# Performance work log

Hardware: AMD Instinct MI355X
Metric: run time of the kernel (lower is better)

## Reference

```python
import jax, jax.numpy as jnp
import numpy as np

B, S, D = 2, 2048, 1024
H = 16
HD = D // H
MLP = 4096
EPS = 1e-5


def _layernorm(x, g, b):
    mu = jnp.mean(x, axis=-1, keepdims=True)
    var = jnp.mean(jnp.square(x - mu), axis=-1, keepdims=True)
    return (x - mu) * jax.lax.rsqrt(var + EPS) * g + b


def setup_inputs() -> dict:
    key = jax.random.key(0)
    ks = jax.random.split(key, 16)
    sd = 0.02
    return {
        "x": jax.random.normal(ks[0], (B, S, D), jnp.float32),
        "dis_attn_mask": jax.random.normal(ks[1], (B, S, S), jnp.float32) * 0.1,
        "cls_attn_mask": jax.random.normal(ks[2], (B, S, S), jnp.float32) * 0.1,
        "wq": jax.random.normal(ks[3], (D, D), jnp.float32) * sd,
        "bq": jnp.zeros((D,), jnp.float32),
        "wk": jax.random.normal(ks[4], (D, D), jnp.float32) * sd,
        "bk": jnp.zeros((D,), jnp.float32),
        "wv": jax.random.normal(ks[5], (D, D), jnp.float32) * sd,
        "bv": jnp.zeros((D,), jnp.float32),
        "ln1_g": jnp.ones((D,), jnp.float32),
        "ln1_b": jnp.zeros((D,), jnp.float32),
        "ln2_g": jnp.ones((D,), jnp.float32),
        "ln2_b": jnp.zeros((D,), jnp.float32),
        "w1": jax.random.normal(ks[6], (D, MLP), jnp.float32) * sd,
        "b1": jnp.zeros((MLP,), jnp.float32),
        "w2": jax.random.normal(ks[7], (MLP, D), jnp.float32) * sd,
        "b2": jnp.zeros((D,), jnp.float32),
    }


def reference(x, dis_attn_mask, cls_attn_mask, wq, bq, wk, bk, wv, bv,
              ln1_g, ln1_b, ln2_g, ln2_b, w1, b1, w2, b2):
    res = x
    h = _layernorm(x, ln1_g, ln1_b)
    q = h @ wq + bq
    k = h @ wk + bk
    v = h @ wv + bv
    # NOTE: original torch code uses .view(B, H, S, HD) on a contiguous
    # [B, S, D] tensor (no transpose); row-major reshape reproduces this.
    q = q.reshape(B, H, S, HD)
    k = k.reshape(B, H, S, HD)
    v = v.reshape(B, H, S, HD)
    w = jnp.einsum('bhsd,bhtd->bhst', q, k) * (HD ** -0.5)
    w = w + dis_attn_mask[:, None] + cls_attn_mask[:, None]
    w = jax.nn.softmax(w, axis=-1)
    h_attn = jnp.einsum('bhst,bhtd->bhsd', w, v).reshape(B, S, D)
    h = h_attn + res
    h = _layernorm(h, ln2_g, ln2_b)
    res2 = h
    h = jax.nn.gelu(h @ w1 + b1, approximate=False) @ w2 + b2
    return h + res2
```

## Files before the change

kernel.cpp:

```cpp
#include <hip/hip_runtime.h>
#include <hip/hip_bf16.h>
#include <math.h>

#define BB 2
#define SS 2048
#define DD 1024
#define HH 16
#define MLPD 4096

typedef __attribute__((ext_vector_type(8))) short bf16x8;
typedef __attribute__((ext_vector_type(4))) float f32x4;
typedef __attribute__((ext_vector_type(4))) unsigned short us4;

static __device__ __forceinline__ float fast_exp2(float x) {
#if __has_builtin(__builtin_amdgcn_exp2f)
  return __builtin_amdgcn_exp2f(x);
#else
  return exp2f(x);
#endif
}
static __device__ __forceinline__ float fast_rcp(float x) {
#if __has_builtin(__builtin_amdgcn_rcpf)
  return __builtin_amdgcn_rcpf(x);
#else
  return 1.0f / x;
#endif
}

static __device__ __forceinline__ unsigned short f2bf(float f) {
  union { float f; unsigned int u; } v; v.f = f;
  unsigned int r = v.u + 0x7fffu + ((v.u >> 16) & 1u);
  return (unsigned short)(r >> 16);
}
static __device__ __forceinline__ float bf2f(unsigned short b) {
  return __uint_as_float(((unsigned int)b) << 16);
}

static __device__ __forceinline__ float gelu_f(float x) {
  float u = x * x;
  float z = x * fmaf(u, 0.0713548162f, 1.59576912f);
  float e = fast_exp2(z * -1.44269504f);
  return x * fast_rcp(1.0f + e);
}

static __device__ __forceinline__ int swz(int row) {
  return (row & 3) ^ ((row >> 2) & 3);
}

__global__ __launch_bounds__(256) void transpose_to_bf16(
    const float* __restrict__ src, unsigned short* __restrict__ dst,
    int K, int N) {
  __shared__ float tile[32][33];
  int t = threadIdx.x;
  int c = t & 31, rl = t >> 5;
  int bx = blockIdx.x, by = blockIdx.y;
#pragma unroll
  for (int i = 0; i < 4; ++i) {
    int row = rl * 4 + i;
    tile[row][c] = src[(size_t)(by * 32 + row) * N + bx * 32 + c];
  }
  __syncthreads();
#pragma unroll
  for (int i = 0; i < 4; ++i) {
    int n = rl * 4 + i;
    dst[(size_t)(bx * 32 + n) * K + by * 32 + c] = f2bf(tile[c][n]);
  }
}

__global__ __launch_bounds__(256) void transpose_qkv(
    const float* __restrict__ wq, const float* __restrict__ wk,
    const float* __restrict__ wv, unsigned short* __restrict__ dst) {
  __shared__ float tile[32][33];
  const float* src = blockIdx.z == 0 ? wq : blockIdx.z == 1 ? wk : wv;
  unsigned short* d = dst + (size_t)blockIdx.z * 1024 * 1024;
  int t = threadIdx.x;
  int c = t & 31, rl = t >> 5;
  int bx = blockIdx.x, by = blockIdx.y;
#pragma unroll
  for (int i = 0; i < 4; ++i) {
    int row = rl * 4 + i;
    tile[row][c] = src[(size_t)(by * 32 + row) * DD + bx * 32 + c];
  }
  __syncthreads();
#pragma unroll
  for (int i = 0; i < 4; ++i) {
    int n = rl * 4 + i;
    d[(size_t)(bx * 32 + n) * DD + by * 32 + c] = f2bf(tile[c][n]);
  }
}

__global__ __launch_bounds__(256) void concat_bias(
    const float* __restrict__ bq, const float* __restrict__ bk,
    const float* __restrict__ bv, float* __restrict__ dst) {
  int i = blockIdx.x * 256 + threadIdx.x;
  if (i < 1024) dst[i] = bq[i];
  else if (i < 2048) dst[i] = bk[i - 1024];
  else if (i < 3072) dst[i] = bv[i - 2048];
}

__global__ __launch_bounds__(256) void mask_prep(
    const float* __restrict__ dis, const float* __restrict__ cls,
    unsigned short* __restrict__ cm) {
  size_t i = ((size_t)blockIdx.x * 256 + threadIdx.x) * 4;
  float4 d = *(const float4*)(dis + i);
  float4 c = *(const float4*)(cls + i);
  us4 o;
  o[0] = f2bf((d.x + c.x) * 1.44269504f);
  o[1] = f2bf((d.y + c.y) * 1.44269504f);
  o[2] = f2bf((d.z + c.z) * 1.44269504f);
  o[3] = f2bf((d.w + c.w) * 1.44269504f);
  *(us4*)(cm + i) = o;
}

template <bool BF_IN, bool ADD>
__global__ __launch_bounds__(256) void ln_bf16(
    const void* __restrict__ in, const float* __restrict__ add,
    const float* __restrict__ g, const float* __restrict__ beta,
    unsigned short* __restrict__ out) {
  int row = blockIdx.x;
  int t = threadIdx.x;
  float x[4];
  if (BF_IN) {
    us4 b4 = *(const us4*)((const unsigned short*)in + (size_t)row * DD + t * 4);
#pragma unroll
    for (int i = 0; i < 4; ++i) x[i] = bf2f(b4[i]);
  } else {
    float4 f4 = *(const float4*)((const float*)in + (size_t)row * DD + t * 4);
    x[0] = f4.x; x[1] = f4.y; x[2] = f4.z; x[3] = f4.w;
  }
  if (ADD) {
    float4 a4 = *(const float4*)(add + (size_t)row * DD + t * 4);
    x[0] += a4.x; x[1] += a4.y; x[2] += a4.z; x[3] += a4.w;
  }
  float s1 = x[0] + x[1] + x[2] + x[3];
  float s2 = x[0] * x[0] + x[1] * x[1] + x[2] * x[2] + x[3] * x[3];
#pragma unroll
  for (int off = 32; off > 0; off >>= 1) {
    s1 += __shfl_down(s1, off);
    s2 += __shfl_down(s2, off);
  }
  __shared__ float sa[4], sb[4];
  int wid = t >> 6;
  if ((t & 63) == 0) { sa[wid] = s1; sb[wid] = s2; }
  __syncthreads();
  s1 = sa[0] + sa[1] + sa[2] + sa[3];
  s2 = sb[0] + sb[1] + sb[2] + sb[3];
  float mean = s1 * (1.0f / 1024.0f);
  float var = s2 * (1.0f / 1024.0f) - mean * mean;
  float rstd = rsqrtf(var + 1e-5f);
  float4 gv = *(const float4*)(g + t * 4);
  float4 bv = *(const float4*)(beta + t * 4);
  us4 o;
  o[0] = f2bf((x[0] - mean) * rstd * gv.x + bv.x);
  o[1] = f2bf((x[1] - mean) * rstd * gv.y + bv.y);
  o[2] = f2bf((x[2] - mean) * rstd * gv.z + bv.z);
  o[3] = f2bf((x[3] - mean) * rstd * gv.w + bv.w);
  *(us4*)(out + (size_t)row * DD + t * 4) = o;
}

template <int BN, bool GELU, bool ADDSRC, bool OUT_BF16, bool SPLIT3>
__global__ __launch_bounds__(256) void gemm_bf16(
    const unsigned short* __restrict__ A, const unsigned short* __restrict__ BT,
    const float* __restrict__ bias, const unsigned short* __restrict__ addsrc,
    void* C0, void* C1, void* C2, int M, int N, int K) {
  constexpr int BJ = BN / 32;
  constexpr int BCH = BN / 64;
  __shared__ __align__(16) unsigned short As[128][32];
  __shared__ __align__(16) unsigned short Bs[BN][32];
  int tid = threadIdx.x;
  int wave = tid >> 6, lane = tid & 63;
  int g = lane >> 4, c16 = lane & 15;
  int m0 = blockIdx.y * 128, n0 = blockIdx.x * BN;
  int wm = (wave >> 1) * 64, wn = (wave & 1) * (BN / 2);
  int lrow = lane >> 2, lq = lane & 3;
  int dq = (lq ^ swz(lrow)) * 8;
  const unsigned short* aS = A + (size_t)(m0 + wave * 32 + lrow) * K + lq * 8;
  unsigned short* aD0 = &As[wave * 32 + lrow][dq];
  unsigned short* aD1 = &As[wave * 32 + 16 + lrow][dq];
  const unsigned short* bS = BT + (size_t)(n0 + wave * (BCH * 16) + lrow) * K + lq * 8;
  unsigned short* bD0 = &Bs[wave * (BCH * 16) + lrow][dq];
  unsigned short* bD1 = &Bs[(wave * (BCH * 16) + 16 + lrow) % BN][dq];
  int vA = (g ^ swz(c16)) * 8;
  const int KI = K / 32;
  const size_t rK = 16 * (size_t)K;

  bf16x8 a0a = *(const bf16x8*)(aS);
  bf16x8 a1a = *(const bf16x8*)(aS + rK);
  bf16x8 b0a = *(const bf16x8*)(bS);
  bf16x8 b1a;
  if constexpr (BCH == 2) b1a = *(const bf16x8*)(bS + rK);
  bf16x8 a0b = *(const bf16x8*)(aS + 32);
  bf16x8 a1b = *(const bf16x8*)(aS + rK + 32);
  bf16x8 b0b = *(const bf16x8*)(bS + 32);
  bf16x8 b1b;
  if constexpr (BCH == 2) b1b = *(const bf16x8*)(bS + rK + 32);

  f32x4 acc[4][BJ] = {};
  for (int kt = 0; kt < KI; kt += 2) {
    __syncthreads();
    *(bf16x8*)aD0 = a0a;
    *(bf16x8*)aD1 = a1a;
    *(bf16x8*)bD0 = b0a;
    if constexpr (BCH == 2) *(bf16x8*)bD1 = b1a;
    __syncthreads();
    if (kt + 2 < KI) {
      int ko = (kt + 2) * 32;
      a0a = *(const bf16x8*)(aS + ko);
      a1a = *(const bf16x8*)(aS + rK + ko);
      b0a = *(const bf16x8*)(bS + ko);
      if constexpr (BCH == 2) b1a = *(const bf16x8*)(bS + rK + ko);
    }
    {
      bf16x8 a[4], b[BJ];
#pragma unroll
      for (int i = 0; i < 4; ++i) a[i] = *(const bf16x8*)&As[wm + i * 16 + c16][vA];
#pragma unroll
      for (int j = 0; j < BJ; ++j) b[j] = *(const bf16x8*)&Bs[wn + j * 16 + c16][vA];
#pragma unroll
      for (int i = 0; i < 4; ++i)
#pragma unroll
        for (int j = 0; j < BJ; ++j)
          acc[i][j] = __builtin_amdgcn_mfma_f32_16x16x32_bf16(a[i], b[j], acc[i][j], 0, 0, 0);
    }
    __syncthreads();
    *(bf16x8*)aD0 = a0b;
    *(bf16x8*)aD1 = a1b;
    *(bf16x8*)bD0 = b0b;
    if constexpr (BCH == 2) *(bf16x8*)bD1 = b1b;
    __syncthreads();
    if (kt + 3 < KI) {
      int ko = (kt + 3) * 32;
      a0b = *(const bf16x8*)(aS + ko);
      a1b = *(const bf16x8*)(aS + rK + ko);
      b0b = *(const bf16x8*)(bS + ko);
      if constexpr (BCH == 2) b1b = *(const bf16x8*)(bS + rK + ko);
    }
    {
      bf16x8 a[4], b[BJ];
#pragma unroll
      for (int i = 0; i < 4; ++i) a[i] = *(const bf16x8*)&As[wm + i * 16 + c16][vA];
#pragma unroll
      for (int j = 0; j < BJ; ++j) b[j] = *(const bf16x8*)&Bs[wn + j * 16 + c16][vA];
#pragma unroll
      for (int i = 0; i < 4; ++i)
#pragma unroll
        for (int j = 0; j < BJ; ++j)
          acc[i][j] = __builtin_amdgcn_mfma_f32_16x16x32_bf16(a[i], b[j], acc[i][j], 0, 0, 0);
    }
  }
  unsigned short* dstb = nullptr;
  int lc0 = 0;
  if (SPLIT3) {
    int which = n0 >> 10;
    dstb = (unsigned short*)(which == 0 ? C0 : which == 1 ? C1 : C2);
    lc0 = n0 & 1023;
  }
#pragma unroll
  for (int j = 0; j < BJ; ++j) {
    int coff = wn + j * 16 + c16;
    float bj = bias[n0 + coff];
#pragma unroll
    for (int i = 0; i < 4; ++i) {
#pragma unroll
      for (int r = 0; r < 4; ++r) {
        int row = m0 + wm + i * 16 + g * 4 + r;
        float cval = acc[i][j][r] + bj;
        if (GELU) cval = gelu_f(cval);
        if (ADDSRC) cval += bf2f(addsrc[(size_t)row * N + n0 + coff]);
        if (SPLIT3) {
          dstb[(size_t)row * 1024 + lc0 + coff] = f2bf(cval);
        } else if (OUT_BF16) {
          ((unsigned short*)C0)[(size_t)row * N + n0 + coff] = f2bf(cval);
        } else {
          ((float*)C0)[(size_t)row * N + n0 + coff] = cval;
        }
      }
    }
  }
}

__global__ __launch_bounds__(512) void attn_mfma(
    const unsigned short* __restrict__ q, const unsigned short* __restrict__ k,
    const unsigned short* __restrict__ v, const unsigned short* __restrict__ cm,
    unsigned short* __restrict__ outO) {
  __shared__ __align__(16) unsigned short Ks[2][64][32];
  __shared__ __align__(16) unsigned short Vt[64][72];
  __shared__ __align__(16) unsigned short Ps[128][72];
  int tid = threadIdx.x;
  int wave = tid >> 6, lane = tid & 63;
  int g = lane >> 4, c16 = lane & 15;
  int qt = blockIdx.x, h = blockIdx.y, b = blockIdx.z;
  int s0 = qt * 128;
  int wr = wave * 16;
  size_t headoff = (size_t)b * SS * DD + (size_t)h * SS * 64;
  const unsigned short* qb = q + headoff;
  const unsigned short* kb = k + headoff;
  const unsigned short* vb = v + headoff;
  const unsigned short* cmb = cm + (size_t)b * SS * SS;

  int kkey = tid >> 3, kseg = tid & 7;
  unsigned short* kdst = &Ks[kseg >> 2][kkey][((kseg & 3) ^ swz(kkey)) * 8];
  const unsigned short* ksrc = kb + (size_t)kkey * 64 + kseg * 8;
  const unsigned short* vsrc = vb + (size_t)lane * 64 + wave * 8;
  int vK = (g ^ swz(c16)) * 8;

  bf16x8 qf0, qf1;
  {
    size_t qrow = (size_t)(s0 + wr + c16) * 64;
    qf0 = *(const bf16x8*)(qb + qrow + g * 8);
    qf1 = *(const bf16x8*)(qb + qrow + 32 + g * 8);
  }
  bf16x8 ones;
#pragma unroll
  for (int j = 0; j < 8; ++j) ones[j] = (short)0x3F80;
  f32x4 o[4] = {};
  f32x4 ol = {};
  const float scale2 = 0.18033688f;

  bf16x8 kreg = *(const bf16x8*)(ksrc);
  bf16x8 vreg = *(const bf16x8*)(vsrc);
  unsigned short cmc[4][4];
#pragma unroll
  for (int t = 0; t < 4; ++t)
#pragma unroll
    for (int r = 0; r < 4; ++r)
      cmc[t][r] = cmb[(size_t)(s0 + wr + g * 4 + r) * SS + t * 16 + c16];

  for (int kt = 0; kt < 32; ++kt) {
    __syncthreads();
    *(bf16x8*)kdst = kreg;
#pragma unroll
    for (int j = 0; j < 8; ++j) Vt[wave * 8 + j][lane] = (unsigned short)vreg[j];
    __syncthreads();

    int ktn = kt + 1 < 32 ? kt + 1 : 31;
    bf16x8 kregN = *(const bf16x8*)(ksrc + (size_t)ktn * 4096);
    bf16x8 vregN = *(const bf16x8*)(vsrc + (size_t)ktn * 4096);
    unsigned short cmN[4][4];
#pragma unroll
    for (int t = 0; t < 4; ++t)
#pragma unroll
      for (int r = 0; r < 4; ++r)
        cmN[t][r] = cmb[(size_t)(s0 + wr + g * 4 + r) * SS + ktn * 64 + t * 16 + c16];

    f32x4 s[4] = {};
#pragma unroll
    for (int t = 0; t < 4; ++t) {
      bf16x8 b0 = *(const bf16x8*)&Ks[0][t * 16 + c16][vK];
      bf16x8 b1 = *(const bf16x8*)&Ks[1][t * 16 + c16][vK];
      s[t] = __builtin_amdgcn_mfma_f32_16x16x32_bf16(qf0, b0, s[t], 0, 0, 0);
      s[t] = __builtin_amdgcn_mfma_f32_16x16x32_bf16(qf1, b1, s[t], 0, 0, 0);
    }
#pragma unroll
    for (int t = 0; t < 4; ++t)
#pragma unroll
      for (int r = 0; r < 4; ++r) {
        float p = fast_exp2(fmaf(s[t][r], scale2, bf2f(cmc[t][r])));
        Ps[wr + g * 4 + r][t * 16 + c16] = (unsigned short)(__float_as_uint(p) >> 16);
      }
#pragma unroll
    for (int ks = 0; ks < 2; ++ks) {
      bf16x8 pa = *(const bf16x8*)&Ps[wr + c16][ks * 32 + g * 8];
#pragma unroll
      for (int t2 = 0; t2 < 4; ++t2) {
        bf16x8 vb8 = *(const bf16x8*)&Vt[t2 * 16 + c16][ks * 32 + g * 8];
        o[t2] = __builtin_amdgcn_mfma_f32_16x16x32_bf16(pa, vb8, o[t2], 0, 0, 0);
      }
      ol = __builtin_amdgcn_mfma_f32_16x16x32_bf16(pa, ones, ol, 0, 0, 0);
    }
    kreg = kregN;
    vreg = vregN;
#pragma unroll
    for (int t = 0; t < 4; ++t)
#pragma unroll
      for (int r = 0; r < 4; ++r) cmc[t][r] = cmN[t][r];
  }
  float inv[4];
#pragma unroll
  for (int r = 0; r < 4; ++r) inv[r] = fast_rcp(ol[r]);
#pragma unroll
  for (int t2 = 0; t2 < 4; ++t2)
#pragma unroll
    for (int r = 0; r < 4; ++r) {
      int srow = s0 + wr + g * 4 + r;
      outO[headoff + (size_t)srow * 64 + t2 * 16 + c16] = f2bf(o[t2][r] * inv[r]);
    }
}

extern "C" void kernel_launch(void* const* d_in, const int* in_sizes, int n_in,
                              void* d_out, int out_size, void* d_ws, size_t ws_size,
                              hipStream_t stream) {
  const float* x    = (const float*)d_in[0];
  const float* dis  = (const float*)d_in[1];
  const float* cls  = (const float*)d_in[2];
  const float* wq   = (const float*)d_in[3];
  const float* bq   = (const float*)d_in[4];
  const float* wk   = (const float*)d_in[5];
  const float* bk   = (const float*)d_in[6];
  const float* wv   = (const float*)d_in[7];
  const float* bv   = (const float*)d_in[8];
  const float* ln1g = (const float*)d_in[9];
  const float* ln1b = (const float*)d_in[10];
  const float* ln2g = (const float*)d_in[11];
  const float* ln2b = (const float*)d_in[12];
  const float* w1   = (const float*)d_in[13];
  const float* b1   = (const float*)d_in[14];
  const float* w2   = (const float*)d_in[15];
  const float* b2   = (const float*)d_in[16];
  float* out = (float*)d_out;
  char* ws = (char*)d_ws;

  unsigned short* qkvwT = (unsigned short*)(ws + 0);
  unsigned short* w1T   = (unsigned short*)(ws + 6291456);
  unsigned short* w2T   = (unsigned short*)(ws + 14680064);
  float*          qkvb  = (float*)(ws + 23068672);
  unsigned short* r1    = (unsigned short*)(ws + 23134208);
  unsigned short* qbuf  = (unsigned short*)(ws + 31522816);
  unsigned short* kbuf  = (unsigned short*)(ws + 39911424);
  unsigned short* vbuf  = (unsigned short*)(ws + 48300032);
  unsigned short* h2    = (unsigned short*)(ws + 56688640);
  unsigned short* cmb   = (unsigned short*)(ws + 65077248);
  unsigned short* mm    = (unsigned short*)(ws + 23134208);
  unsigned short* h1 = r1;
  unsigned short* attnO = r1;

  const int rows = BB * SS;

  transpose_qkv<<<dim3(DD / 32, DD / 32, 3), 256, 0, stream>>>(wq, wk, wv, qkvwT);
  transpose_to_bf16<<<dim3(MLPD / 32, DD / 32), 256, 0, stream>>>(w1, w1T, DD, MLPD);
  transpose_to_bf16<<<dim3(DD / 32, MLPD / 32), 256, 0, stream>>>(w2, w2T, MLPD, DD);
  concat_bias<<<12, 256, 0, stream>>>(bq, bk, bv, qkvb);
  mask_prep<<<8192, 256, 0, stream>>>(dis, cls, cmb);

  ln_bf16<false, false><<<rows, 256, 0, stream>>>(x, nullptr, ln1g, ln1b, h1);

  gemm_bf16<128, false, false, true, true><<<dim3(3072 / 128, rows / 128), 256, 0, stream>>>(
      h1, qkvwT, qkvb, nullptr, qbuf, kbuf, vbuf, rows, 3072, DD);

  attn_mfma<<<dim3(SS / 128, HH, BB), 512, 0, stream>>>(qbuf, kbuf, vbuf, cmb, attnO);

  ln_bf16<true, true><<<rows, 256, 0, stream>>>(attnO, x, ln2g, ln2b, h2);

  gemm_bf16<128, true, false, true, false><<<dim3(MLPD / 128, rows / 128), 256, 0, stream>>>(
      h2, w1T, b1, nullptr, mm, nullptr, nullptr, rows, MLPD, DD);

  gemm_bf16<64, false, true, false, false><<<dim3(DD / 64, rows / 128), 256, 0, stream>>>(
      mm, w2T, b2, h2, out, nullptr, nullptr, rows, DD, MLPD);
}
```

Baseline: 399.6 us.

## Add 256x256 async-LDS pipelined GEMM for QKV and MLP-up projections

Measured after the change: 400.1 us. No clear change (+0.1%).

```diff
diff --git a/kernel.cpp b/kernel.cpp
--- a/kernel.cpp
+++ b/kernel.cpp
@@ -45,6 +45,12 @@
 
 static __device__ __forceinline__ int swz(int row) {
   return (row & 3) ^ ((row >> 2) & 3);
+}
+
+static __device__ __forceinline__ void async16(const unsigned short* g, unsigned short* l) {
+  __builtin_amdgcn_global_load_lds(
+      (const __attribute__((address_space(1))) unsigned int*)g,
+      (__attribute__((address_space(3))) unsigned int*)l, 16, 0, 0);
 }
 
 __global__ __launch_bounds__(256) void transpose_to_bf16(
@@ -279,6 +285,133 @@
   }
 }
 
+#define VMW(n) asm volatile("s_waitcnt vmcnt(" #n ")" ::: "memory")
+#define BARX() do { asm volatile("" ::: "memory"); \
+                    __builtin_amdgcn_s_barrier(); \
+                    asm volatile("" ::: "memory"); } while (0)
+
+template <bool GELU, bool SPLIT3>
+__global__ __launch_bounds__(512, 2) void gemm256(
+    const unsigned short* __restrict__ A, const unsigned short* __restrict__ BT,
+    const float* __restrict__ bias, void* C0, void* C1, void* C2,
+    int N, int K) {
+  __shared__ __align__(16) char lds[2][2][2][16384];
+  int tid = threadIdx.x;
+  int lane = tid & 63, w = tid >> 6;
+  int g = lane >> 4, c16 = lane & 15;
+  int wm16 = (w >> 2) << 4;
+  int wn16 = (w & 3) << 4;
+  int m0 = blockIdx.y << 8, n0 = blockIdx.x << 8;
+
+  int st0 = tid >> 6, ci0 = tid & 63;
+  int cp0 = ci0 ^ (((ci0 >> 5) & 1) << 1);
+  int sr0 = ((st0 >> 1) << 4) + (cp0 >> 2);
+  int sk0 = ((st0 & 1) << 5) + ((cp0 & 3) << 3);
+  size_t soff = (size_t)sr0 * K + sk0;
+
+  auto stage = [&](int op, int h, int tt, int d) {
+    const unsigned short* base = (op == 0 ? A : BT);
+    int row0 = (op == 0 ? m0 : n0) + (h << 7);
+    const unsigned short* src = base + (size_t)row0 * K + (tt << 6) + soff;
+    unsigned short* dst = (unsigned short*)&lds[op][d][h][tid * 16];
+    async16(src, dst);
+    async16(src + ((size_t)K << 6), dst + 4096);
+  };
+
+  auto foff = [&](int r, int ke) -> int {
+    int stt = ((r >> 4) << 1) + (ke >> 5);
+    int loc = ((r & 15) << 6) + ((ke & 31) << 1);
+    return (stt << 10) + (loc ^ (((r >> 3) & 1) << 5));
+  };
+  int offA[4][2], offB[2][2];
+#pragma unroll
+  for (int ii = 0; ii < 4; ++ii)
+#pragma unroll
+    for (int ks = 0; ks < 2; ++ks)
+      offA[ii][ks] = foff(ii * 32 + wm16 + c16, ks * 32 + g * 8);
+#pragma unroll
+  for (int jj = 0; jj < 2; ++jj)
+#pragma unroll
+    for (int ks = 0; ks < 2; ++ks)
+      offB[jj][ks] = foff(jj * 64 + wn16 + c16, ks * 32 + g * 8);
+
+  f32x4 acc[8][4] = {};
+
+#define PHASE(IH, JH, D, STAGE_STMT, WAIT_STMT) do {                          \
+    const char* pa = &lds[0][D][IH][0];                                       \
+    const char* pb = &lds[1][D][JH][0];                                       \
+    bf16x8 af[4][2], bfr[2][2];                                               \
+    _Pragma("unroll") for (int ii = 0; ii < 4; ++ii)                          \
+      _Pragma("unroll") for (int ks = 0; ks < 2; ++ks)                        \
+        af[ii][ks] = *(const bf16x8*)(pa + offA[ii][ks]);                     \
+    _Pragma("unroll") for (int jj = 0; jj < 2; ++jj)                          \
+      _Pragma("unroll") for (int ks = 0; ks < 2; ++ks)                        \
+        bfr[jj][ks] = *(const bf16x8*)(pb + offB[jj][ks]);                    \
+    STAGE_STMT;                                                               \
+    WAIT_STMT;                                                                \
+    BARX();                                                                   \
+    __builtin_amdgcn_s_setprio(1);                                            \
+    _Pragma("unroll") for (int ii = 0; ii < 4; ++ii)                          \
+      _Pragma("unroll") for (int jj = 0; jj < 2; ++jj) {                      \
+        acc[(IH)*4+ii][(JH)*2+jj] = __builtin_amdgcn_mfma_f32_16x16x32_bf16(  \
+            af[ii][0], bfr[jj][0], acc[(IH)*4+ii][(JH)*2+jj], 0, 0, 0);       \
+        acc[(IH)*4+ii][(JH)*2+jj] = __builtin_amdgcn_mfma_f32_16x16x32_bf16(  \
+            af[ii][1], bfr[jj][1], acc[(IH)*4+ii][(JH)*2+jj], 0, 0, 0);       \
+      }                                                                       \
+    __builtin_amdgcn_s_setprio(0);                                            \
+    BARX();                                                                   \
+  } while (0)
+
+  stage(0, 0, 0, 0);
+  stage(1, 0, 0, 0);
+  stage(1, 1, 0, 0);
+  stage(0, 1, 0, 0);
+  stage(0, 0, 1, 1);
+  stage(1, 0, 1, 1);
+  VMW(6);
+  BARX();
+
+  const int KT = K >> 6;
+  for (int kt = 0; kt < KT; ++kt) {
+    int d = kt & 1, dn = d ^ 1;
+    int t1 = kt + 1 < KT ? kt + 1 : KT - 1;
+    int t2 = kt + 2 < KT ? kt + 2 : KT - 1;
+    PHASE(0, 0, d, stage(1, 1, t1, dn), (void)0);
+    PHASE(0, 1, d, stage(0, 1, t1, dn), VMW(8));
+    PHASE(1, 0, d, stage(0, 0, t2, d), (void)0);
+    PHASE(1, 1, d, stage(1, 0, t2, d), VMW(6));
+  }
+#undef PHASE
+
+  unsigned short* dstb = nullptr;
+  int lc0 = 0;
+  if (SPLIT3) {
+    int which = n0 >> 10;
+    dstb = (unsigned short*)(which == 0 ? C0 : which == 1 ? C1 : C2);
+    lc0 = n0 & 1023;
+  }
+#pragma unroll
+  for (int i = 0; i < 8; ++i) {
+#pragma unroll
+    for (int j = 0; j < 4; ++j) {
+      int row_b = m0 + ((i >> 2) << 7) + ((i & 3) << 5) + wm16 + (g << 2);
+      int colp = ((j >> 1) << 7) + ((j & 1) << 6) + wn16 + c16;
+      float bj = bias[n0 + colp];
+#pragma unroll
+      for (int r = 0; r < 4; ++r) {
+        float cv = acc[i][j][r] + bj;
+        if (GELU) cv = gelu_f(cv);
+        int row = row_b + r;
+        if (SPLIT3) {
+          dstb[(size_t)row * 1024 + lc0 + colp] = f2bf(cv);
+        } else {
+          ((unsigned short*)C0)[(size_t)row * N + n0 + colp] = f2bf(cv);
+        }
+      }
+    }
+  }
+}
+
 __global__ __launch_bounds__(512) void attn_mfma(
     const unsigned short* __restrict__ q, const unsigned short* __restrict__ k,
     const unsigned short* __restrict__ v, const unsigned short* __restrict__ cm,
@@ -434,15 +567,15 @@
 
   ln_bf16<false, false><<<rows, 256, 0, stream>>>(x, nullptr, ln1g, ln1b, h1);
 
-  gemm_bf16<128, false, false, true, true><<<dim3(3072 / 128, rows / 128), 256, 0, stream>>>(
-      h1, qkvwT, qkvb, nullptr, qbuf, kbuf, vbuf, rows, 3072, DD);
+  gemm256<false, true><<<dim3(3072 / 256, rows / 256), 512, 0, stream>>>(
+      h1, qkvwT, qkvb, qbuf, kbuf, vbuf, 3072, DD);
 
   attn_mfma<<<dim3(SS / 128, HH, BB), 512, 0, stream>>>(qbuf, kbuf, vbuf, cmb, attnO);
 
   ln_bf16<true, true><<<rows, 256, 0, stream>>>(attnO, x, ln2g, ln2b, h2);
 
-  gemm_bf16<128, true, false, true, false><<<dim3(MLPD / 128, rows / 128), 256, 0, stream>>>(
-      h2, w1T, b1, nullptr, mm, nullptr, nullptr, rows, MLPD, DD);
+  gemm256<true, false><<<dim3(MLPD / 256, rows / 256), 512, 0, stream>>>(
+      h2, w1T, b1, mm, nullptr, nullptr, MLPD, DD);
 
   gemm_bf16<64, false, true, false, false><<<dim3(DD / 64, rows / 128), 256, 0, stream>>>(
       mm, w2T, b2, h2, out, nullptr, nullptr, rows, DD, MLPD);
```
